# Kernel optimization log

Hardware: AMD Instinct MI355X
Metric: run time of the kernel (lower is better)

Reference implementation:

```python
import jax, jax.numpy as jnp
import numpy as np

EPS = 1e-5

def layer_norm(x, g, b):
    m = x.mean(-1, keepdims=True)
    v = ((x - m) ** 2).mean(-1, keepdims=True)
    return (x - m) / jnp.sqrt(v + EPS) * g + b

def multihead(qn, kn, vn, Wq, Wk, Wv, causal):
    # Wq/Wk/Wv: [H, E, D]; per-head projections stacked over H (matches per-head Linear loop)
    Q = jnp.einsum('ble,hed->bhld', qn, Wq)
    K = jnp.einsum('bme,hed->bhmd', kn, Wk)
    V = jnp.einsum('bme,hed->bhmd', vn, Wv)
    scale = Q.shape[-1] ** -0.5
    s = jnp.einsum('bhld,bhmd->bhlm', Q, K) * scale
    if causal:
        L, M = s.shape[-2], s.shape[-1]
        mask = jnp.tril(jnp.ones((L, M), dtype=bool))
        s = jnp.where(mask, s, -jnp.inf)
    w = jax.nn.softmax(s, axis=-1)
    o = jnp.einsum('bhlm,bhmd->bhld', w, V)
    return o.mean(axis=1)  # heads are AVERAGED, not concatenated


def setup_inputs() -> dict:
    key = jax.random.key(0)
    ks = jax.random.split(key, 16)
    B, L, E, H, D, FW = 4, 2048, 512, 8, 512, 4
    std = 0.02
    inp = {
        'q': jax.random.normal(ks[0], (B, L, E), jnp.float32),
        'k': jax.random.normal(ks[1], (B, L, E), jnp.float32),
        'v': jax.random.normal(ks[2], (B, L, E), jnp.float32),
        'Wq_s': jax.random.normal(ks[3], (H, E, D), jnp.float32) * std,
        'Wk_s': jax.random.normal(ks[4], (H, E, D), jnp.float32) * std,
        'Wv_s': jax.random.normal(ks[5], (H, E, D), jnp.float32) * std,
        'Wq_c': jax.random.normal(ks[6], (H, E, D), jnp.float32) * std,
        'Wk_c': jax.random.normal(ks[7], (H, E, D), jnp.float32) * std,
        'Wv_c': jax.random.normal(ks[8], (H, E, D), jnp.float32) * std,
        'W1': jax.random.normal(ks[9], (E, FW * E), jnp.float32) * std,
        'b1': jnp.zeros((FW * E,), jnp.float32),
        'W2': jax.random.normal(ks[10], (FW * E, E), jnp.float32) * std,
        'b2': jnp.zeros((E,), jnp.float32),
        'g1': jnp.ones((E,), jnp.float32), 'be1': jnp.zeros((E,), jnp.float32),
        'g2': jnp.ones((E,), jnp.float32), 'be2': jnp.zeros((E,), jnp.float32),
        'g3': jnp.ones((E,), jnp.float32), 'be3': jnp.zeros((E,), jnp.float32),
    }
    return inp


def reference(q, k, v, Wq_s, Wk_s, Wv_s, Wq_c, Wk_c, Wv_c, W1, b1, W2, b2,
              g1, be1, g2, be2, g3, be3):
    # pre-norm causal self-attn (head_size == n_embd, heads averaged)
    q = q + multihead(layer_norm(q, g1, be1), layer_norm(q, g1, be1), layer_norm(q, g1, be1),
                      Wq_s, Wk_s, Wv_s, causal=True)
    # pre-norm cross-attn: only queries are normed; k, v used raw
    q = q + multihead(layer_norm(q, g2, be2), k, v, Wq_c, Wk_c, Wv_c, causal=False)
    # FFN
    h = layer_norm(q, g3, be3)
    h = jax.nn.relu(h @ W1 + b1) @ W2 + b2
    return q + h
```

## Files before the change

kernel.cpp:

```cpp
#include <hip/hip_runtime.h>
#include <cstdint>


typedef __bf16 bf16;
typedef __bf16 bf16x8 __attribute__((ext_vector_type(8)));
typedef float f32x4 __attribute__((ext_vector_type(4)));
typedef int i32x4 __attribute__((ext_vector_type(4)));
typedef int i32x8 __attribute__((ext_vector_type(8)));
typedef unsigned short u16;

static constexpr int Bb = 4, Ls = 2048, Es = 512, Hh = 8, Dd = 512, Ff = 2048;
static constexpr long BL = (long)Bb * Ls;
static constexpr int BIG = 1 << 30;

#define DEV __device__ __forceinline__

DEV u16 f2bf(float x) {
  unsigned u = __float_as_uint(x);
  return (u16)((u + 0x7fffu + ((u >> 16) & 1u)) >> 16);
}

DEV void async16(const void* gp, void* lp) {
  __builtin_amdgcn_global_load_lds(
      (const __attribute__((address_space(1))) void*)gp,
      (__attribute__((address_space(3))) void*)lp, 16, 0, 0);
}

template <int OUT, int SM, int IN8, int O8, bool BIAS, bool RELU, bool CAUSAL, bool RESID,
          bool TRI, bool DIAG>
__global__ __launch_bounds__(256) void gemm128(
    const void* __restrict__ A, const void* __restrict__ Bt, void* __restrict__ Cout,
    const float* __restrict__ bias, const float* __restrict__ resid,
    float* __restrict__ rsum,
    int M, int N, int K, int lda, int ldb, int ldc, int ldct, int tz,
    long sA, int dA, long sAi, int mA, int dAi,
    long sB, int mB, long sB2, int dB,
    long sC, int dC, long sCi, int mC, float alpha) {
  int xt, yt;
  if (TRI) {
    const int bx = blockIdx.x;
    int y = (int)((sqrtf(8.0f * bx + 1.0f) - 1.0f) * 0.5f);
    while ((y + 1) * (y + 2) / 2 <= bx) ++y;
    while (y * (y + 1) / 2 > bx) --y;
    yt = y; xt = bx - y * (y + 1) / 2;
  } else {
    xt = blockIdx.x; yt = blockIdx.y;
    if (DIAG) yt = (int)((unsigned)(yt + blockIdx.z) % gridDim.y);
  }
  const int m0 = yt * 128, n0 = xt * 128;
  int Keff = K;
  if (CAUSAL && SM == 2) { int kl = m0 + 128; Keff = kl < K ? kl : K; }

  const int z = blockIdx.z;
  const char* Ab = (const char*)A + (long)(z / dA) * sA + (long)((z % mA) / dAi) * sAi;
  const char* Bbp = (const char*)Bt + (long)(z % mB) * sB + (long)(z / dB) * sB2;
  char* Cb = (char*)Cout + (long)(z / dC) * sC + (long)(z % mC) * sCi;
  float* RS = (SM != 0) ? (rsum + (long)z * M) : nullptr;
  const int zc = z % mC;

  constexpr int ES = IN8 ? 1 : 2;
  constexpr int KS = IN8 ? 128 : 64;
  const long lasA = (long)lda * ES, lasB = (long)ldb * ES;

  __shared__ char As[16384];
  __shared__ char Bs[16384];

  const int tid = threadIdx.x;
  const int lane = tid & 63;
  const int quad = lane >> 4, r = lane & 15;
  const int wave = tid >> 6;
  const int wm = (wave >> 1) * 64, wn = (wave & 1) * 64;

  f32x4 acc[4][4];
  const f32x4 zero = {0.f, 0.f, 0.f, 0.f};
#pragma unroll
  for (int i = 0; i < 4; ++i)
#pragma unroll
    for (int j = 0; j < 4; ++j) acc[i][j] = zero;

  for (int k0 = 0; k0 < Keff; k0 += KS) {
#pragma unroll
    for (int i = 0; i < 4; ++i) {
      const int c = i * 256 + tid, row = c >> 3;
      const int s = (c & 7) ^ (row & 7);
      async16(Ab + (long)(m0 + row) * lasA + ((long)k0 * ES + s * 16), As + c * 16);
    }
#pragma unroll
    for (int i = 0; i < 4; ++i) {
      const int c = i * 256 + tid, row = c >> 3;
      const int s = (c & 7) ^ (row & 7);
      async16(Bbp + (long)(n0 + row) * lasB + ((long)k0 * ES + s * 16), Bs + c * 16);
    }
    asm volatile("s_waitcnt vmcnt(0)" ::: "memory");
    __syncthreads();

    if (IN8) {
      i32x8 af[4], bw[4];
#pragma unroll
      for (int t = 0; t < 4; ++t) {
        const int Ra = wm + t * 16 + r;
        const char* pa = As + Ra * 128;
        i32x4 alo = *(const i32x4*)(pa + (((2 * quad) ^ (Ra & 7)) * 16));
        i32x4 ahi = *(const i32x4*)(pa + (((2 * quad + 1) ^ (Ra & 7)) * 16));
        af[t] = __builtin_shufflevector(alo, ahi, 0, 1, 2, 3, 4, 5, 6, 7);
        const int Rb = wn + t * 16 + r;
        const char* pb = Bs + Rb * 128;
        i32x4 blo = *(const i32x4*)(pb + (((2 * quad) ^ (Rb & 7)) * 16));
        i32x4 bhi = *(const i32x4*)(pb + (((2 * quad + 1) ^ (Rb & 7)) * 16));
        bw[t] = __builtin_shufflevector(blo, bhi, 0, 1, 2, 3, 4, 5, 6, 7);
      }
#pragma unroll
      for (int i = 0; i < 4; ++i)
#pragma unroll
        for (int j = 0; j < 4; ++j)
          acc[i][j] = __builtin_amdgcn_mfma_scale_f32_16x16x128_f8f6f4(
              af[i], bw[j], acc[i][j], 0, 0, 0, 0x7f7f7f7f, 0, 0x7f7f7f7f);
    } else {
#pragma unroll
      for (int u = 0; u < 2; ++u) {
        bf16x8 af[4], bw[4];
#pragma unroll
        for (int t = 0; t < 4; ++t) {
          const int Ra = wm + t * 16 + r;
          af[t] = *(const bf16x8*)(As + Ra * 128 + (((u * 4 + quad) ^ (Ra & 7)) * 16));
          const int Rb = wn + t * 16 + r;
          bw[t] = *(const bf16x8*)(Bs + Rb * 128 + (((u * 4 + quad) ^ (Rb & 7)) * 16));
        }
#pragma unroll
        for (int i = 0; i < 4; ++i)
#pragma unroll
          for (int j = 0; j < 4; ++j)
            acc[i][j] = __builtin_amdgcn_mfma_f32_16x16x32_bf16(af[i], bw[j], acc[i][j], 0, 0, 0);
      }
    }
    __syncthreads();
  }

#pragma unroll
  for (int i = 0; i < 4; ++i) {
    const int rowb = m0 + wm + i * 16 + quad * 4;
    if (SM == 1) {
      float rpart[4] = {0.f, 0.f, 0.f, 0.f};
#pragma unroll
      for (int j = 0; j < 4; ++j) {
        const int col = n0 + wn + j * 16 + r;
#pragma unroll
        for (int t = 0; t < 4; ++t) {
          float p = __expf(acc[i][j][t] * alpha);
          if (CAUSAL && col > rowb + t) p = 0.f;
          rpart[t] += p;
          if (O8) {
            int w8 = __builtin_amdgcn_cvt_pk_fp8_f32(p, p, 0, false);
            Cb[(long)(rowb + t) * ldc + col] = (char)(w8 & 0xff);
          } else {
            ((u16*)Cb)[(long)(rowb + t) * ldc + col] = f2bf(p);
          }
        }
      }
#pragma unroll
      for (int t = 0; t < 4; ++t) {
        rpart[t] += __shfl_xor(rpart[t], 1);
        rpart[t] += __shfl_xor(rpart[t], 2);
        rpart[t] += __shfl_xor(rpart[t], 4);
        rpart[t] += __shfl_xor(rpart[t], 8);
      }
      if (r == 0) {
#pragma unroll
        for (int t = 0; t < 4; ++t) atomicAdd(RS + rowb + t, rpart[t]);
      }
      continue;
    }
    float rinv[4];
    if (SM == 2) {
#pragma unroll
      for (int t = 0; t < 4; ++t) rinv[t] = alpha / RS[rowb + t];
    }
#pragma unroll
    for (int j = 0; j < 4; ++j) {
      const int col = n0 + wn + j * 16 + r;
      float v[4];
#pragma unroll
      for (int t = 0; t < 4; ++t)
        v[t] = (SM == 2) ? acc[i][j][t] * rinv[t] : acc[i][j][t] * alpha;
      if (BIAS) {
        const float bb = bias[col];
#pragma unroll
        for (int t = 0; t < 4; ++t) v[t] += bb;
      }
      if (RELU) {
#pragma unroll
        for (int t = 0; t < 4; ++t) v[t] = fmaxf(v[t], 0.f);
      }
      if (OUT == 0) {
        float* C = (float*)Cb;
#pragma unroll
        for (int t = 0; t < 4; ++t) {
          long idx = (long)(rowb + t) * ldc + col;
          float o = v[t];
          if (RESID) o += resid[idx];
          C[idx] = o;
        }
      } else {
        if (zc >= tz) {
          if (O8) {
            int w8 = __builtin_amdgcn_cvt_pk_fp8_f32(v[0], v[1], 0, false);
            w8 = __builtin_amdgcn_cvt_pk_fp8_f32(v[2], v[3], w8, true);
            *(int*)(Cb + (long)col * ldct + rowb) = w8;
          } else {
            ushort4 p;
            p.x = f2bf(v[0]); p.y = f2bf(v[1]); p.z = f2bf(v[2]); p.w = f2bf(v[3]);
            *(ushort4*)((u16*)Cb + (long)col * ldct + rowb) = p;
          }
        } else {
#pragma unroll
          for (int t = 0; t < 4; ++t) {
            if (O8) {
              int w8 = __builtin_amdgcn_cvt_pk_fp8_f32(v[t], v[t], 0, false);
              Cb[(long)(rowb + t) * ldc + col] = (char)(w8 & 0xff);
            } else {
              ((u16*)Cb)[(long)(rowb + t) * ldc + col] = f2bf(v[t]);
            }
          }
        }
      }
    }
  }
}

template <int F8>
__global__ __launch_bounds__(256) void ln_kernel(
    const float* __restrict__ x, const float* __restrict__ g, const float* __restrict__ be,
    void* __restrict__ y, float* __restrict__ xcopy, int nrows) {
  const int wave = threadIdx.x >> 6, lane = threadIdx.x & 63;
  const long row = (long)blockIdx.x * 4 + wave;
  const float4* xr = (const float4*)(x + row * 512);
  float4 v0 = xr[lane], v1 = xr[lane + 64];
  if (xcopy) {
    float4* c = (float4*)(xcopy + row * 512);
    c[lane] = v0; c[lane + 64] = v1;
  }
  float s = v0.x + v0.y + v0.z + v0.w + v1.x + v1.y + v1.z + v1.w;
#pragma unroll
  for (int o = 32; o >= 1; o >>= 1) s += __shfl_xor(s, o);
  const float m = s * (1.0f / 512.0f);
  float d = (v0.x - m) * (v0.x - m) + (v0.y - m) * (v0.y - m) + (v0.z - m) * (v0.z - m) +
            (v0.w - m) * (v0.w - m) + (v1.x - m) * (v1.x - m) + (v1.y - m) * (v1.y - m) +
            (v1.z - m) * (v1.z - m) + (v1.w - m) * (v1.w - m);
#pragma unroll
  for (int o = 32; o >= 1; o >>= 1) d += __shfl_xor(d, o);
  const float rstd = rsqrtf(d * (1.0f / 512.0f) + 1e-5f);
  const float4* gv = (const float4*)g;
  const float4* bv = (const float4*)be;
  float4 g0 = gv[lane], g1 = gv[lane + 64], b0 = bv[lane], b1 = bv[lane + 64];
  float n0 = (v0.x - m) * rstd * g0.x + b0.x, n1 = (v0.y - m) * rstd * g0.y + b0.y;
  float n2 = (v0.z - m) * rstd * g0.z + b0.z, n3 = (v0.w - m) * rstd * g0.w + b0.w;
  float n4 = (v1.x - m) * rstd * g1.x + b1.x, n5 = (v1.y - m) * rstd * g1.y + b1.y;
  float n6 = (v1.z - m) * rstd * g1.z + b1.z, n7 = (v1.w - m) * rstd * g1.w + b1.w;
  if (F8) {
    char* yr = (char*)y + row * 512;
    int w0 = __builtin_amdgcn_cvt_pk_fp8_f32(n0, n1, 0, false);
    w0 = __builtin_amdgcn_cvt_pk_fp8_f32(n2, n3, w0, true);
    int w1 = __builtin_amdgcn_cvt_pk_fp8_f32(n4, n5, 0, false);
    w1 = __builtin_amdgcn_cvt_pk_fp8_f32(n6, n7, w1, true);
    *(int*)(yr + 4 * lane) = w0;
    *(int*)(yr + 256 + 4 * lane) = w1;
  } else {
    uint2 o0, o1;
    o0.x = (unsigned)f2bf(n0) | ((unsigned)f2bf(n1) << 16);
    o0.y = (unsigned)f2bf(n2) | ((unsigned)f2bf(n3) << 16);
    o1.x = (unsigned)f2bf(n4) | ((unsigned)f2bf(n5) << 16);
    o1.y = (unsigned)f2bf(n6) | ((unsigned)f2bf(n7) << 16);
    uint2* yr = (uint2*)((u16*)y + row * 512);
    yr[lane] = o0; yr[lane + 64] = o1;
  }
}

__global__ __launch_bounds__(256) void cvt_fp8_kernel(const float* __restrict__ x,
                                                      char* __restrict__ y, long n) {
  long i = ((long)blockIdx.x * 256 + threadIdx.x) * 8;
  if (i >= n) return;
  float4 a = *(const float4*)(x + i), b = *(const float4*)(x + i + 4);
  int w0 = __builtin_amdgcn_cvt_pk_fp8_f32(a.x, a.y, 0, false);
  w0 = __builtin_amdgcn_cvt_pk_fp8_f32(a.z, a.w, w0, true);
  int w1 = __builtin_amdgcn_cvt_pk_fp8_f32(b.x, b.y, 0, false);
  w1 = __builtin_amdgcn_cvt_pk_fp8_f32(b.z, b.w, w1, true);
  int2 o; o.x = w0; o.y = w1;
  *(int2*)(y + i) = o;
}

__global__ __launch_bounds__(256) void zero_kernel(float* __restrict__ p) {
  long i = ((long)blockIdx.x * 256 + threadIdx.x) * 4;
  const float4 z4 = {0.f, 0.f, 0.f, 0.f};
  *(float4*)(p + i) = z4;
}

__global__ __launch_bounds__(256) void transpose6(
    const float* __restrict__ s0, const float* __restrict__ s1, const float* __restrict__ s2,
    const float* __restrict__ s3, const float* __restrict__ s4, const float* __restrict__ s5,
    char* __restrict__ out) {
  __shared__ float t[32][33];
  const int set = blockIdx.z >> 3, head = blockIdx.z & 7;
  const float* in = set == 0 ? s0 : set == 1 ? s1 : set == 2 ? s2
                   : set == 3 ? s3 : set == 4 ? s4 : s5;
  const long sW = (long)Es * Dd;
  in += (long)head * sW;
  char* o = out + ((long)set * Hh + head) * sW;
  const int c0 = blockIdx.x * 32, r0 = blockIdx.y * 32;
  const int tx = threadIdx.x & 31, ty = threadIdx.x >> 5;
#pragma unroll
  for (int i = 0; i < 32; i += 8) t[ty + i][tx] = in[(long)(r0 + ty + i) * Dd + (c0 + tx)];
  __syncthreads();
#pragma unroll
  for (int i = 0; i < 32; i += 8) {
    float xv = t[tx][ty + i] * 64.0f;
    o[(long)(c0 + ty + i) * Es + (r0 + tx)] =
        (char)(__builtin_amdgcn_cvt_pk_fp8_f32(xv, xv, 0, false) & 0xff);
  }
}

__global__ __launch_bounds__(256) void transpose_cvt8(const float* __restrict__ in,
                                                      char* __restrict__ out, int R, int C) {
  __shared__ float t[32][33];
  const int c0 = blockIdx.x * 32, r0 = blockIdx.y * 32;
  const int tx = threadIdx.x & 31, ty = threadIdx.x >> 5;
#pragma unroll
  for (int i = 0; i < 32; i += 8) t[ty + i][tx] = in[(long)(r0 + ty + i) * C + (c0 + tx)];
  __syncthreads();
#pragma unroll
  for (int i = 0; i < 32; i += 8) {
    float xv = t[tx][ty + i] * 64.0f;
    out[(long)(c0 + ty + i) * R + (r0 + tx)] =
        (char)(__builtin_amdgcn_cvt_pk_fp8_f32(xv, xv, 0, false) & 0xff);
  }
}

__global__ __launch_bounds__(256) void reduce8b_kernel(const u16* __restrict__ O,
                                                       float* __restrict__ acc) {
  const long n = (long)Ls * Dd;
  const u16* Ob = O + (long)blockIdx.y * 8 * n;
  float* ab = acc + (long)blockIdx.y * (long)Ls * Es;
  long i = ((long)blockIdx.x * 256 + threadIdx.x) * 8;
  float s[8] = {0.f, 0.f, 0.f, 0.f, 0.f, 0.f, 0.f, 0.f};
#pragma unroll
  for (int h = 0; h < 8; ++h) {
    bf16x8 t = *(const bf16x8*)(Ob + (long)h * n + i);
#pragma unroll
    for (int e = 0; e < 8; ++e) s[e] += (float)t[e];
  }
  float4 a0 = *(const float4*)(ab + i);
  float4 a1 = *(const float4*)(ab + i + 4);
  a0.x += s[0]; a0.y += s[1]; a0.z += s[2]; a0.w += s[3];
  a1.x += s[4]; a1.y += s[5]; a1.z += s[6]; a1.w += s[7];
  *(float4*)(ab + i) = a0;
  *(float4*)(ab + i + 4) = a1;
}

__global__ __launch_bounds__(256) void finalize_kernel(const float* __restrict__ slabs,
                                                       const float* __restrict__ resid,
                                                       const float* __restrict__ b2,
                                                       float* __restrict__ out) {
  const long SL = (long)BL * Es;
  long i = ((long)blockIdx.x * 256 + threadIdx.x) * 4;
  float4 a0 = *(const float4*)(slabs + i);
  float4 a1 = *(const float4*)(slabs + SL + i);
  float4 a2 = *(const float4*)(slabs + 2 * SL + i);
  float4 a3 = *(const float4*)(slabs + 3 * SL + i);
  float4 rr = *(const float4*)(resid + i);
  float4 bb = *(const float4*)(b2 + (int)(i & 511));
  float4 o;
  o.x = a0.x + a1.x + a2.x + a3.x + rr.x + bb.x;
  o.y = a0.y + a1.y + a2.y + a3.y + rr.y + bb.y;
  o.z = a0.z + a1.z + a2.z + a3.z + rr.z + bb.z;
  o.w = a0.w + a1.w + a2.w + a3.w + rr.w + bb.w;
  *(float4*)(out + i) = o;
}

extern "C" void kernel_launch(void* const* d_in, const int* in_sizes, int n_in,
                              void* d_out, int out_size, void* d_ws, size_t ws_size,
                              hipStream_t stream) {
  const float* q = (const float*)d_in[0];
  const float* k = (const float*)d_in[1];
  const float* v = (const float*)d_in[2];
  const float* Wq_s = (const float*)d_in[3];
  const float* Wk_s = (const float*)d_in[4];
  const float* Wv_s = (const float*)d_in[5];
  const float* Wq_c = (const float*)d_in[6];
  const float* Wk_c = (const float*)d_in[7];
  const float* Wv_c = (const float*)d_in[8];
  const float* W1 = (const float*)d_in[9];
  const float* b1 = (const float*)d_in[10];
  const float* W2 = (const float*)d_in[11];
  const float* b2 = (const float*)d_in[12];
  const float* g1 = (const float*)d_in[13];
  const float* be1 = (const float*)d_in[14];
  const float* g2 = (const float*)d_in[15];
  const float* be2 = (const float*)d_in[16];
  const float* g3 = (const float*)d_in[17];
  const float* be3 = (const float*)d_in[18];

  char* w = (char*)d_ws;
  size_t off = 0;
  auto alloc = [&](size_t bytes) -> char* {
    char* p = w + off;
    off += (bytes + 255) & ~(size_t)255;
    return p;
  };
  const long sW = (long)Es * Dd;
  const long sQ = (long)Ls * Dd;
  const long sS = (long)Ls * Ls;
  const long sBE = (long)Ls * Es;

  u16* Wqst = (u16*)alloc((size_t)Hh * sW * 2);
  u16* Wkst = (u16*)alloc((size_t)Hh * sW * 2);
  u16* Wvst = (u16*)alloc((size_t)Hh * sW * 2);
  u16* Wqct = (u16*)alloc((size_t)Hh * sW * 2);
  u16* Wkct = (u16*)alloc((size_t)Hh * sW * 2);
  u16* Wvct = (u16*)alloc((size_t)Hh * sW * 2);
  u16* W1t = (u16*)alloc((size_t)Es * Ff * 2);
  u16* W2t = (u16*)alloc((size_t)Es * Ff * 2);
  u16* qn = (u16*)alloc((size_t)BL * Es * 2);
  u16* knb = (u16*)alloc((size_t)BL * Es * 2);
  u16* vnb = (u16*)alloc((size_t)BL * Es * 2);
  char* QKV = alloc((size_t)Hh * sQ * 2);
  char* KVx = alloc((size_t)Hh * sQ * 2);
  u16* Vtb = (u16*)alloc((size_t)Hh * sQ * 2);
  char* Sb = alloc((size_t)Hh * sS * 2);
  float* acc1 = (float*)alloc((size_t)BL * Es * 4);
  u16* hbuf = (u16*)alloc((size_t)BL * Ff * 2);
  (void)KVx; (void)Vtb; (void)Wkst; (void)Wvst; (void)Wqct; (void)Wkct; (void)Wvct;
  char* QKVp = QKV;
  float* accF = (float*)Sb;
  float* rsum = (float*)W1t;
  char* Wq8 = (char*)Wqst;
  char* qn8 = (char*)qn;
  char* W1t8 = (char*)W1t;
  char* W2t8 = (char*)W2t;
  char* h8 = (char*)hbuf;
  const long tstr = (long)BL * Es * 2;
  (void)in_sizes; (void)n_in; (void)out_size; (void)ws_size;

  const dim3 blk(256);
  transpose6<<<dim3(Dd / 32, Es / 32, 48), blk, 0, stream>>>(Wq_s, Wk_s, Wv_s, Wq_c, Wk_c, Wv_c, Wq8);
  cvt_fp8_kernel<<<dim3((unsigned)(BL * Es / 2048)), blk, 0, stream>>>(k, (char*)knb, BL * Es);
  cvt_fp8_kernel<<<dim3((unsigned)(BL * Es / 2048)), blk, 0, stream>>>(v, (char*)vnb, BL * Es);
  zero_kernel<<<dim3(8 * Hh * Ls / 1024), blk, 0, stream>>>(rsum);

  ln_kernel<1><<<dim3((unsigned)(BL / 4)), blk, 0, stream>>>(q, g1, be1, qn8, acc1, (int)BL);

  const float scl = 0.044194173824159216f;
  const float sclS = scl / 4096.0f;
  const float aPV = 0.125f / 64.0f;
  const float aW = 1.0f / 64.0f;
  const float* np = nullptr;

  for (int p = 0; p < 2; ++p) {
    const char* qp8 = qn8 + (long)p * 2 * sBE;
    float* rsS = rsum + (long)p * 16 * Ls;
    gemm128<1, 0, 1, 1, false, false, false, false, false, false><<<dim3(4, 16, 48), blk, 0, stream>>>(
        qp8, Wq8, QKVp, np, np, nullptr, Ls, Dd, Es, Es, Es, Dd, Ls, 16,
        sBE, 24, 0, 24, 8,
        sW, 24, 0, 1,
        24 * sQ, 24, sQ, 24,
        1.0f);
    gemm128<1, 1, 1, 1, false, false, true, false, true, false><<<dim3(136, 1, 16), blk, 0, stream>>>(
        QKVp, QKVp + 8 * sQ, Sb, np, np, rsS, Ls, Ls, Dd, Dd, Dd, Ls, Ls, BIG,
        24 * sQ, 8, sQ, 8, 1,
        sQ, 8, 24 * sQ, 8,
        8 * sS, 8, sS, 8,
        sclS);
    gemm128<1, 2, 1, 0, false, false, true, false, false, true><<<dim3(4, 16, 16), blk, 0, stream>>>(
        Sb, QKVp + 16 * sQ, hbuf, np, np, rsS, Ls, Dd, Ls, Ls, Ls, Dd, Ls, BIG,
        8 * sS, 8, sS, 8, 1,
        sQ, 8, 24 * sQ, 8,
        8 * sQ * 2, 8, sQ * 2, 8,
        aPV);
    reduce8b_kernel<<<dim3(512, 2), blk, 0, stream>>>(hbuf, acc1 + (long)p * 2 * sBE);
  }

  ln_kernel<1><<<dim3((unsigned)(BL / 4)), blk, 0, stream>>>(acc1, g2, be2, qn8, nullptr, (int)BL);

  for (int p = 0; p < 2; ++p) {
    const char* qp8 = qn8 + (long)p * 2 * sBE;
    float* rsS = rsum + (long)(32 + p * 16) * Ls;
    gemm128<1, 0, 1, 1, false, false, false, false, false, false><<<dim3(4, 16, 48), blk, 0, stream>>>(
        qp8, Wq8 + 24 * sW, QKVp, np, np, nullptr, Ls, Dd, Es, Es, Es, Dd, Ls, 16,
        sBE, 24, tstr, 24, 8,
        sW, 24, 0, 1,
        24 * sQ, 24, sQ, 24,
        1.0f);
    gemm128<1, 1, 1, 1, false, false, false, false, false, false><<<dim3(16, 16, 16), blk, 0, stream>>>(
        QKVp, QKVp + 8 * sQ, Sb, np, np, rsS, Ls, Ls, Dd, Dd, Dd, Ls, Ls, BIG,
        24 * sQ, 8, sQ, 8, 1,
        sQ, 8, 24 * sQ, 8,
        8 * sS, 8, sS, 8,
        sclS);
    gemm128<1, 2, 1, 0, false, false, false, false, false, false><<<dim3(4, 16, 16), blk, 0, stream>>>(
        Sb, QKVp + 16 * sQ, hbuf, np, np, rsS, Ls, Dd, Ls, Ls, Ls, Dd, Ls, BIG,
        8 * sS, 8, sS, 8, 1,
        sQ, 8, 24 * sQ, 8,
        8 * sQ * 2, 8, sQ * 2, 8,
        aPV);
    reduce8b_kernel<<<dim3(512, 2), blk, 0, stream>>>(hbuf, acc1 + (long)p * 2 * sBE);
  }

  transpose_cvt8<<<dim3(Ff / 32, Es / 32, 1), blk, 0, stream>>>(W1, W1t8, Es, Ff);
  transpose_cvt8<<<dim3(Es / 32, Ff / 32, 1), blk, 0, stream>>>(W2, W2t8, Ff, Es);

  ln_kernel<1><<<dim3((unsigned)(BL / 4)), blk, 0, stream>>>(acc1, g3, be3, qn8, nullptr, (int)BL);
  gemm128<1, 0, 1, 1, true, true, false, false, false, false><<<dim3(Ff / 128, (unsigned)(BL / 128), 1), blk, 0, stream>>>(
      qn8, W1t8, h8, b1, np, nullptr, (int)BL, Ff, Es, Es, Es, Ff, Ff, BIG,
      0, 1, 0, 1, 1,
      0, 1, 0, 1,
      0, 1, 0, 1, aW);
  gemm128<0, 0, 1, 0, false, false, false, false, false, false><<<dim3(Es / 128, (unsigned)(BL / 128), 4), blk, 0, stream>>>(
      h8, W2t8, accF, np, np, nullptr, (int)BL, Es, 512, Ff, Ff, Es, Es, BIG,
      512, 1, 0, 1, 1,
      0, 1, 512, 1,
      (long)BL * Es * 4, 1, 0, 1,
      aW);
  finalize_kernel<<<dim3((unsigned)(BL * Es / 1024)), blk, 0, stream>>>(accF, acc1, b2, (float*)d_out);
}
```

Measured before the change: 852.2 us.

## Replace head-reduction and split-K finalize kernels with float atomic accumulation in GEMM epilogue

Adds an atomic-add output mode to the GEMM epilogue. The PV GEMMs now add each head's output straight into the fp32 residual accumulator instead of writing bf16 per-head slabs that a separate reduce kernel summed. The split-K W2 GEMM likewise atomically accumulates into the output, which a new prefill kernel seeds with residual plus bias. This removes two reduction kernels and their intermediate buffer traffic, at the cost of atomic contention (8 heads or 4 splits per element) and a summation order that is no longer deterministic.

```diff
diff --git a/kernel.cpp b/kernel.cpp
--- a/kernel.cpp
+++ b/kernel.cpp
@@ -191,7 +191,12 @@
 #pragma unroll
         for (int t = 0; t < 4; ++t) v[t] = fmaxf(v[t], 0.f);
       }
-      if (OUT == 0) {
+      if (OUT == 2) {
+        float* C = (float*)Cb;
+#pragma unroll
+        for (int t = 0; t < 4; ++t)
+          atomicAdd(&C[(long)(rowb + t) * ldc + col], v[t]);
+      } else if (OUT == 0) {
         float* C = (float*)Cb;
 #pragma unroll
         for (int t = 0; t < 4; ++t) {
@@ -334,44 +339,14 @@
   }
 }
 
-__global__ __launch_bounds__(256) void reduce8b_kernel(const u16* __restrict__ O,
-                                                       float* __restrict__ acc) {
-  const long n = (long)Ls * Dd;
-  const u16* Ob = O + (long)blockIdx.y * 8 * n;
-  float* ab = acc + (long)blockIdx.y * (long)Ls * Es;
-  long i = ((long)blockIdx.x * 256 + threadIdx.x) * 8;
-  float s[8] = {0.f, 0.f, 0.f, 0.f, 0.f, 0.f, 0.f, 0.f};
-#pragma unroll
-  for (int h = 0; h < 8; ++h) {
-    bf16x8 t = *(const bf16x8*)(Ob + (long)h * n + i);
-#pragma unroll
-    for (int e = 0; e < 8; ++e) s[e] += (float)t[e];
-  }
-  float4 a0 = *(const float4*)(ab + i);
-  float4 a1 = *(const float4*)(ab + i + 4);
-  a0.x += s[0]; a0.y += s[1]; a0.z += s[2]; a0.w += s[3];
-  a1.x += s[4]; a1.y += s[5]; a1.z += s[6]; a1.w += s[7];
-  *(float4*)(ab + i) = a0;
-  *(float4*)(ab + i + 4) = a1;
-}
-
-__global__ __launch_bounds__(256) void finalize_kernel(const float* __restrict__ slabs,
-                                                       const float* __restrict__ resid,
-                                                       const float* __restrict__ b2,
-                                                       float* __restrict__ out) {
-  const long SL = (long)BL * Es;
+__global__ __launch_bounds__(256) void prefill_kernel(const float* __restrict__ acc,
+                                                      const float* __restrict__ b2,
+                                                      float* __restrict__ out) {
   long i = ((long)blockIdx.x * 256 + threadIdx.x) * 4;
-  float4 a0 = *(const float4*)(slabs + i);
-  float4 a1 = *(const float4*)(slabs + SL + i);
-  float4 a2 = *(const float4*)(slabs + 2 * SL + i);
-  float4 a3 = *(const float4*)(slabs + 3 * SL + i);
-  float4 rr = *(const float4*)(resid + i);
+  float4 a = *(const float4*)(acc + i);
   float4 bb = *(const float4*)(b2 + (int)(i & 511));
   float4 o;
-  o.x = a0.x + a1.x + a2.x + a3.x + rr.x + bb.x;
-  o.y = a0.y + a1.y + a2.y + a3.y + rr.y + bb.y;
-  o.z = a0.z + a1.z + a2.z + a3.z + rr.z + bb.z;
-  o.w = a0.w + a1.w + a2.w + a3.w + rr.w + bb.w;
+  o.x = a.x + bb.x; o.y = a.y + bb.y; o.z = a.z + bb.z; o.w = a.w + bb.w;
   *(float4*)(out + i) = o;
 }
 
@@ -429,7 +404,6 @@
   u16* hbuf = (u16*)alloc((size_t)BL * Ff * 2);
   (void)KVx; (void)Vtb; (void)Wkst; (void)Wvst; (void)Wqct; (void)Wkct; (void)Wvct;
   char* QKVp = QKV;
-  float* accF = (float*)Sb;
   float* rsum = (float*)W1t;
   char* Wq8 = (char*)Wqst;
   char* qn8 = (char*)qn;
@@ -468,13 +442,12 @@
         sQ, 8, 24 * sQ, 8,
         8 * sS, 8, sS, 8,
         sclS);
-    gemm128<1, 2, 1, 0, false, false, true, false, false, true><<<dim3(4, 16, 16), blk, 0, stream>>>(
-        Sb, QKVp + 16 * sQ, hbuf, np, np, rsS, Ls, Dd, Ls, Ls, Ls, Dd, Ls, BIG,
+    gemm128<2, 2, 1, 0, false, false, true, false, false, true><<<dim3(4, 16, 16), blk, 0, stream>>>(
+        Sb, QKVp + 16 * sQ, acc1 + (long)p * 2 * sBE, np, np, rsS, Ls, Dd, Ls, Ls, Ls, Dd, Ls, BIG,
         8 * sS, 8, sS, 8, 1,
         sQ, 8, 24 * sQ, 8,
-        8 * sQ * 2, 8, sQ * 2, 8,
+        sBE * 4, 8, 0, 8,
         aPV);
-    reduce8b_kernel<<<dim3(512, 2), blk, 0, stream>>>(hbuf, acc1 + (long)p * 2 * sBE);
   }
 
   ln_kernel<1><<<dim3((unsigned)(BL / 4)), blk, 0, stream>>>(acc1, g2, be2, qn8, nullptr, (int)BL);
@@ -494,29 +467,28 @@
         sQ, 8, 24 * sQ, 8,
         8 * sS, 8, sS, 8,
         sclS);
-    gemm128<1, 2, 1, 0, false, false, false, false, false, false><<<dim3(4, 16, 16), blk, 0, stream>>>(
-        Sb, QKVp + 16 * sQ, hbuf, np, np, rsS, Ls, Dd, Ls, Ls, Ls, Dd, Ls, BIG,
+    gemm128<2, 2, 1, 0, false, false, false, false, false, false><<<dim3(4, 16, 16), blk, 0, stream>>>(
+        Sb, QKVp + 16 * sQ, acc1 + (long)p * 2 * sBE, np, np, rsS, Ls, Dd, Ls, Ls, Ls, Dd, Ls, BIG,
         8 * sS, 8, sS, 8, 1,
         sQ, 8, 24 * sQ, 8,
-        8 * sQ * 2, 8, sQ * 2, 8,
+        sBE * 4, 8, 0, 8,
         aPV);
-    reduce8b_kernel<<<dim3(512, 2), blk, 0, stream>>>(hbuf, acc1 + (long)p * 2 * sBE);
   }
 
   transpose_cvt8<<<dim3(Ff / 32, Es / 32, 1), blk, 0, stream>>>(W1, W1t8, Es, Ff);
   transpose_cvt8<<<dim3(Es / 32, Ff / 32, 1), blk, 0, stream>>>(W2, W2t8, Ff, Es);
 
   ln_kernel<1><<<dim3((unsigned)(BL / 4)), blk, 0, stream>>>(acc1, g3, be3, qn8, nullptr, (int)BL);
+  prefill_kernel<<<dim3((unsigned)(BL * Es / 1024)), blk, 0, stream>>>(acc1, b2, (float*)d_out);
   gemm128<1, 0, 1, 1, true, true, false, false, false, false><<<dim3(Ff / 128, (unsigned)(BL / 128), 1), blk, 0, stream>>>(
       qn8, W1t8, h8, b1, np, nullptr, (int)BL, Ff, Es, Es, Es, Ff, Ff, BIG,
       0, 1, 0, 1, 1,
       0, 1, 0, 1,
       0, 1, 0, 1, aW);
-  gemm128<0, 0, 1, 0, false, false, false, false, false, false><<<dim3(Es / 128, (unsigned)(BL / 128), 4), blk, 0, stream>>>(
-      h8, W2t8, accF, np, np, nullptr, (int)BL, Es, 512, Ff, Ff, Es, Es, BIG,
+  gemm128<2, 0, 1, 0, false, false, false, false, false, false><<<dim3(Es / 128, (unsigned)(BL / 128), 4), blk, 0, stream>>>(
+      h8, W2t8, (float*)d_out, np, np, nullptr, (int)BL, Es, 512, Ff, Ff, Es, Es, BIG,
       512, 1, 0, 1, 1,
       0, 1, 512, 1,
-      (long)BL * Es * 4, 1, 0, 1,
+      0, 1, 0, 1,
       aW);
-  finalize_kernel<<<dim3((unsigned)(BL * Es / 1024)), blk, 0, stream>>>(accF, acc1, b2, (float*)d_out);
-}
+}
```

Result: slower. 973.1 us (+14.2%).
